# Kernel optimization log

Hardware: AMD Instinct MI355X
Metric: run time of the kernel (lower is better)

The kernel has to match this reference:

```python
import jax, jax.numpy as jnp
import numpy as np

N, E = 40000, 640000
D_IN, D_EDGE, D_HID, D_MSP, D_OUT, L = 16, 8, 128, 256, 4, 2


def _mlp(h, w1, b1, w2, b2):
    # Linear -> ReLU -> Linear
    return jnp.maximum(h @ w1 + b1, 0.0) @ w2 + b2


def setup_inputs() -> dict:
    key = jax.random.key(0)
    ks = jax.random.split(key, 16)
    s = 0.05
    return {
        "x": jax.random.normal(ks[0], (N, D_IN), jnp.float32),
        "edge_attr": jax.random.normal(ks[1], (E, D_EDGE), jnp.float32),
        "edge_index": jax.random.randint(ks[2], (2, E), 0, N, jnp.int32),
        "node_w": jax.random.normal(ks[3], (D_IN, D_HID), jnp.float32) * s,
        "node_b": jnp.zeros((D_HID,), jnp.float32),
        "edge_w": jax.random.normal(ks[4], (D_EDGE, D_HID), jnp.float32) * s,
        "edge_b": jnp.zeros((D_HID,), jnp.float32),
        "msg_w1": jax.random.normal(ks[5], (L, D_HID, D_MSP), jnp.float32) * s,
        "msg_b1": jnp.zeros((L, D_MSP), jnp.float32),
        "msg_w2": jax.random.normal(ks[6], (L, D_MSP, D_HID), jnp.float32) * s,
        "msg_b2": jnp.zeros((L, D_HID), jnp.float32),
        "upd_w1": jax.random.normal(ks[7], (L, D_HID, D_MSP), jnp.float32) * s,
        "upd_b1": jnp.zeros((L, D_MSP), jnp.float32),
        "upd_w2": jax.random.normal(ks[8], (L, D_MSP, D_HID), jnp.float32) * s,
        "upd_b2": jnp.zeros((L, D_HID), jnp.float32),
        "final_w": jax.random.normal(ks[9], (D_HID, D_OUT), jnp.float32) * s,
        "final_b": jnp.zeros((D_OUT,), jnp.float32),
    }


def reference(x, edge_attr, edge_index, node_w, node_b, edge_w, edge_b,
              msg_w1, msg_b1, msg_w2, msg_b2,
              upd_w1, upd_b1, upd_w2, upd_b2, final_w, final_b):
    n_nodes = x.shape[0]
    src, dst = edge_index[0], edge_index[1]  # x_j gathered from src, aggregated onto dst
    # n_lin_layers == 1: single lift layers (dropout is identity in eval)
    h = x @ node_w + node_b                  # [N, 128]
    ea = edge_attr @ edge_w + edge_b         # [E, 128]
    # mean-aggregation degree, zero-degree clamped to 1 (PyG scatter-mean behavior)
    deg = jax.ops.segment_sum(jnp.ones_like(dst, x.dtype), dst, num_segments=n_nodes)
    deg = jnp.maximum(deg, 1.0)[:, None]
    xs = [h]
    for l in range(msg_w1.shape[0]):
        # message: mlp_message(x_j) + mlp_message(edge_attr)
        m = _mlp(h[src], msg_w1[l], msg_b1[l], msg_w2[l], msg_b2[l]) \
            + _mlp(ea, msg_w1[l], msg_b1[l], msg_w2[l], msg_b2[l])
        aggr = jax.ops.segment_sum(m, dst, num_segments=n_nodes) / deg
        # update: mlp_update(x) + mlp_update(aggr_out)
        h = _mlp(h, upd_w1[l], upd_b1[l], upd_w2[l], upd_b2[l]) \
            + _mlp(aggr, upd_w1[l], upd_b1[l], upd_w2[l], upd_b2[l])
        xs.append(h)
    # JumpingKnowledge(mode='max'): elementwise max across layer outputs
    h = jnp.max(jnp.stack(xs, axis=0), axis=0)
    return h @ final_w + final_b  # [N, 4]
```

## Files before the change

kernel.cpp:

```cpp
#include <hip/hip_runtime.h>

#define NN 40000
#define EE 640000
#define MAXT 58752
#define SCAN_B 157

typedef unsigned short u16;
typedef unsigned int u32;
typedef unsigned long long u64;
typedef __attribute__((ext_vector_type(8))) short short8;
typedef __attribute__((ext_vector_type(4))) float f32x4;
typedef __attribute__((ext_vector_type(16))) float f32x16;

__device__ __forceinline__ float bf2f(u16 b){ u32 u=((u32)b)<<16; float f; __builtin_memcpy(&f,&u,4); return f; }
__device__ __forceinline__ u16 f2bf(float f){ u32 u; __builtin_memcpy(&u,&f,4); u = (u + 0x7fffu + ((u>>16)&1u))>>16; return (u16)u; }

#define MFMA __builtin_amdgcn_mfma_f32_16x16x32_bf16
#define MFMA32 __builtin_amdgcn_mfma_f32_32x32x16_bf16

__global__ __launch_bounds__(256)
void packall_kernel(const float* __restrict__ mw1, const float* __restrict__ mw2,
                    const float* __restrict__ uw1, const float* __restrict__ uw2,
                    u16* __restrict__ dm1, u16* __restrict__ dm2,
                    u16* __restrict__ du1, u16* __restrict__ du2){
    int idx = blockIdx.x*blockDim.x + threadIdx.x;
    if (idx >= 4*65536) return;
    int a = idx >> 16, rem = idx & 65535;
    int l = rem >> 15, e = rem & 32767;
    const float* src; u16* dst;
    if (a == 0){ src = mw1; dst = dm1; }
    else if (a == 1){ src = uw1; dst = du1; }
    else if (a == 2){ src = mw2; dst = dm2; }
    else { src = uw2; dst = du2; }
    float v = src[l*32768 + e];
    int o;
    if (a < 2){ int k = e >> 8, n = e & 255;
        o = (((k>>5)*16 + (n>>4))*64 + ((k>>3)&3)*16 + (n&15))*8 + (k&7); }
    else {      int k = e >> 7, n = e & 127;
        o = (((k>>5)*8 + (n>>4))*64 + ((k>>3)&3)*16 + (n&15))*8 + (k&7); }
    dst[l*32768 + o] = f2bf(v);
}

#define SMEM_BYTES 151552

template<int MODE>
__global__ __launch_bounds__(512, 1)
void mlp_kernel(const u16* __restrict__ xa, const u16* __restrict__ xb,
                const u16* __restrict__ w1fg, const float* __restrict__ b1g,
                const u16* __restrict__ w2fg, const float* __restrict__ b2g,
                u16* __restrict__ out16, u16* __restrict__ hmaxb, int ntiles)
{
    extern __shared__ char smem[];
    short8* w1f = (short8*)smem;
    short8* w2f = (short8*)(smem + 65536);
    u16* stg_all = (u16*)(smem + 131072);

    const int tid = threadIdx.x;
    {
        const short8* s1 = (const short8*)w1fg;
        const short8* s2 = (const short8*)w2fg;
        #pragma unroll
        for (int i = 0; i < 8; ++i) w1f[tid + i*512] = s1[tid + i*512];
        #pragma unroll
        for (int i = 0; i < 8; ++i) w2f[tid + i*512] = s2[tid + i*512];
    }
    __syncthreads();

    const int wave = tid >> 6, lane = tid & 63;
    const int g = lane >> 4, c16 = lane & 15;
    u16* stg = stg_all + wave*1280;

    const int wid0 = blockIdx.x*8 + wave;
    const int nwaves = gridDim.x*8;

    for (int t = wid0; t < ntiles; t += nwaves) {
        short8 a[2][4];
        if (MODE == 0) {
            #pragma unroll
            for (int sub = 0; sub < 2; ++sub){
                int r = t*32 + sub*16 + c16;
                #pragma unroll
                for (int kt = 0; kt < 4; ++kt)
                    a[sub][kt] = *(const short8*)(xa + r*128 + kt*32 + g*8);
            }
        } else {
            int r = t*16 + c16;
            #pragma unroll
            for (int kt = 0; kt < 4; ++kt){
                a[0][kt] = *(const short8*)(xa + r*128 + kt*32 + g*8);
                a[1][kt] = *(const short8*)(xb + r*128 + kt*32 + g*8);
            }
        }

        f32x4 oacc[2][8];
        #pragma unroll
        for (int s = 0; s < 2; ++s)
            #pragma unroll
            for (int o = 0; o < 8; ++o) oacc[s][o] = (f32x4){0.f,0.f,0.f,0.f};

        #pragma unroll
        for (int ct = 0; ct < 16; ++ct){
            float bv = b1g[ct*16 + c16];
            f32x4 acc0 = {bv,bv,bv,bv}, acc1 = acc0;
            #pragma unroll
            for (int kt = 0; kt < 4; ++kt){
                short8 b = w1f[(kt*16 + ct)*64 + lane];
                acc0 = MFMA(a[0][kt], b, acc0, 0, 0, 0);
                acc1 = MFMA(a[1][kt], b, acc1, 0, 0, 0);
            }
            int colw = (ct & 1)*16 + c16;
            #pragma unroll
            for (int i = 0; i < 4; ++i){
                int row = g*4 + i;
                stg[row*40 + colw]      = f2bf(fmaxf(acc0[i], 0.f));
                stg[(16+row)*40 + colw] = f2bf(fmaxf(acc1[i], 0.f));
            }
            if (ct & 1){
                int kt2 = ct >> 1;
                short8 a20 = *(const short8*)(stg + c16*40 + g*8);
                short8 a21 = *(const short8*)(stg + (16 + c16)*40 + g*8);
                #pragma unroll
                for (int oc = 0; oc < 8; ++oc){
                    short8 b = w2f[(kt2*8 + oc)*64 + lane];
                    oacc[0][oc] = MFMA(a20, b, oacc[0][oc], 0, 0, 0);
                    oacc[1][oc] = MFMA(a21, b, oacc[1][oc], 0, 0, 0);
                }
            }
        }

        if (MODE == 0) {
            #pragma unroll
            for (int s = 0; s < 2; ++s){
                int rbase = t*32 + s*16 + g*4;
                #pragma unroll
                for (int oc = 0; oc < 8; ++oc){
                    int col = oc*16 + c16; float bb = b2g[col];
                    #pragma unroll
                    for (int i = 0; i < 4; ++i)
                        out16[(rbase + i)*128 + col] = f2bf(oacc[s][oc][i] + bb);
                }
            }
        } else {
            int rbase = t*16 + g*4;
            #pragma unroll
            for (int oc = 0; oc < 8; ++oc){
                int col = oc*16 + c16; float bb2 = 2.f*b2g[col];
                #pragma unroll
                for (int i = 0; i < 4; ++i){
                    float v = oacc[0][oc][i] + oacc[1][oc][i] + bb2;
                    int idx = (rbase + i)*128 + col;
                    float hm = bf2f(hmaxb[idx]);
                    hmaxb[idx] = f2bf(fmaxf(hm, v));
                    out16[idx] = f2bf(v);
                }
            }
        }
    }
}

__global__ __launch_bounds__(512, 1)
void edgeh_kernel(const u16* __restrict__ sea, const u16* __restrict__ tnode,
                  const u16* __restrict__ tne, const int* __restrict__ sbase,
                  const float* __restrict__ W1p, const float* __restrict__ b1p,
                  u16* __restrict__ aggrH)
{
    __shared__ short8 w1f[8*64];
    const int tid = threadIdx.x;
    if (tid < 8*64){
        int cb = tid >> 6, lane = tid & 63, half = lane >> 5, c = lane & 31;
        short8 v = (short8){0,0,0,0,0,0,0,0};
        if (half == 0){
            #pragma unroll
            for (int j = 0; j < 8; ++j) v[j] = (short)f2bf(W1p[j*256 + cb*32 + c]);
        } else {
            v[0] = (short)f2bf(b1p[cb*32 + c]);
        }
        w1f[tid] = v;
    }
    __syncthreads();

    const int wave = tid >> 6, lane = tid & 63;
    const int half = lane >> 5, c32 = lane & 31;
    const int wid0 = blockIdx.x*8 + wave;
    const int nwaves = gridDim.x*8;
    const short8 z = (short8){0,0,0,0,0,0,0,0};
    f32x16 zf16;
    #pragma unroll
    for (int i = 0; i < 16; ++i) zf16[i] = 0.f;

    for (int t = wid0; t < MAXT; t += nwaves){
        u16 tv = tne[t];
        int ne = tv & 0x7fff;
        if (ne == 0) continue;
        bool multi = (tv & 0x8000) != 0;
        int node = tnode[t];
        int sb   = sbase[t];

        bool val = c32 < ne;
        short8 a = z;
        if (half == 0){
            int e = sb + c32; if (e > EE-1) e = EE-1;
            short8 t0 = *(const short8*)(sea + (size_t)e*8);
            a = val ? t0 : z;
        } else {
            a[0] = val ? (short)0x3F80 : (short)0;
        }

        u64 base = (u64)(uintptr_t)(aggrH + (size_t)node*256);
        #pragma unroll
        for (int cb = 0; cb < 8; ++cb){
            short8 b = w1f[cb*64 + lane];
            f32x16 h = MFMA32(a, b, zf16, 0, 0, 0);
            float p0 = fmaxf(h[0],0.f) + fmaxf(h[1],0.f)
                     + fmaxf(h[2],0.f) + fmaxf(h[3],0.f);
            float p1 = fmaxf(h[4],0.f) + fmaxf(h[5],0.f)
                     + fmaxf(h[6],0.f) + fmaxf(h[7],0.f);
            float p2 = fmaxf(h[8],0.f) + fmaxf(h[9],0.f)
                     + fmaxf(h[10],0.f) + fmaxf(h[11],0.f);
            float p3 = fmaxf(h[12],0.f) + fmaxf(h[13],0.f)
                     + fmaxf(h[14],0.f) + fmaxf(h[15],0.f);
            float p = (p0 + p1) + (p2 + p3);
            p += __shfl_xor(p, 32, 64);
            float ph = __shfl_xor(p, 1, 64);
            if (half == 0 && !(c32 & 1)){
                u32 pk;
                asm("v_cvt_pk_bf16_f32 %0, %1, %2" : "=v"(pk) : "v"(p), "v"(ph));
                u64 addr = base + (u64)((cb*32 + c32)*2);
                if (multi){
                    asm volatile("global_atomic_pk_add_bf16 %0, %1, off"
                                 :: "v"(addr), "v"(pk) : "memory");
                } else {
                    *(u32*)(uintptr_t)addr = pk;
                }
            }
        }
    }
}

#define P2_SMEM 135168
__global__ __launch_bounds__(512, 1)
void p2_kernel(const u16* __restrict__ aggrH, const u16* __restrict__ w2fg,
               const float* __restrict__ b2g, const int* __restrict__ deg,
               u16* __restrict__ aggr_bf)
{
    extern __shared__ char smem[];
    short8* w2f = (short8*)smem;
    u16* ostg_all = (u16*)(smem + 65536);
    const int tid = threadIdx.x;
    {
        const short8* s2 = (const short8*)w2fg;
        #pragma unroll
        for (int i = 0; i < 8; ++i) w2f[tid + i*512] = s2[tid + i*512];
    }
    __syncthreads();

    const int wave = tid >> 6, lane = tid & 63;
    const int g = lane >> 4, c16 = lane & 15;
    u16* ostg = ostg_all + wave*(32*136);
    const int wid0 = blockIdx.x*8 + wave;
    const int nwaves = gridDim.x*8;
    const int ntiles = NN/32;

    for (int t = wid0; t < ntiles; t += nwaves){
        short8 a[2][8];
        #pragma unroll
        for (int sub = 0; sub < 2; ++sub){
            int r = t*32 + sub*16 + c16;
            #pragma unroll
            for (int kt = 0; kt < 8; ++kt)
                a[sub][kt] = *(const short8*)(aggrH + (size_t)r*256 + kt*32 + g*8);
        }
        f32x4 acc[2][8];
        #pragma unroll
        for (int s = 0; s < 2; ++s)
            #pragma unroll
            for (int o = 0; o < 8; ++o) acc[s][o] = (f32x4){0.f,0.f,0.f,0.f};
        #pragma unroll
        for (int kt = 0; kt < 8; ++kt){
            #pragma unroll
            for (int oc = 0; oc < 8; ++oc){
                short8 b = w2f[(kt*8 + oc)*64 + lane];
                acc[0][oc] = MFMA(a[0][kt], b, acc[0][oc], 0, 0, 0);
                acc[1][oc] = MFMA(a[1][kt], b, acc[1][oc], 0, 0, 0);
            }
        }
        #pragma unroll
        for (int s = 0; s < 2; ++s){
            int rbase = t*32 + s*16 + g*4;
            float dinv[4]; float tf[4];
            #pragma unroll
            for (int i = 0; i < 4; ++i){
                int d = deg[rbase + i];
                tf[i] = (d > 0) ? 1.f : 0.f;
                dinv[i] = 1.f / (float)((d < 1) ? 1 : d);
            }
            #pragma unroll
            for (int oc = 0; oc < 8; ++oc){
                int col = oc*16 + c16; float bb = b2g[col];
                #pragma unroll
                for (int i = 0; i < 4; ++i){
                    float v = acc[s][oc][i]*dinv[i] + tf[i]*bb;
                    ostg[(s*16 + g*4 + i)*136 + col] = f2bf(v);
                }
            }
        }
        #pragma unroll
        for (int j = 0; j < 8; ++j){
            int flat = j*64 + lane;
            int row = flat >> 4, chunk = flat & 15;
            short8 v = *(const short8*)(ostg + row*136 + chunk*8);
            *(short8*)(aggr_bf + (size_t)(t*32 + row)*128 + chunk*8) = v;
        }
    }
}

__global__ __launch_bounds__(512)
void csr_kernel(const u16* __restrict__ mhb, const u16* __restrict__ ssrc,
                const int* __restrict__ offs, const int* __restrict__ deg,
                u16* __restrict__ aggr_bf)
{
    int w = (int)((blockIdx.x*blockDim.x + threadIdx.x) >> 6);
    int lane = threadIdx.x & 63;
    if (w >= NN) return;
    int o0 = offs[w], dn = deg[w];
    const u32* mh32 = (const u32*)mhb;
    float pl = 0.f, ph = 0.f;
    int k = 0;
    for (; k + 8 <= dn; k += 8){
        u32 v[8];
        #pragma unroll
        for (int j = 0; j < 8; ++j){
            int sc = ssrc[o0 + k + j];
            v[j] = mh32[(size_t)sc*64 + lane];
        }
        #pragma unroll
        for (int j = 0; j < 8; ++j){
            pl += bf2f((u16)(v[j] & 0xffffu));
            ph += bf2f((u16)(v[j] >> 16));
        }
    }
    for (; k < dn; ++k){
        int sc = ssrc[o0+k];
        u32 v = mh32[(size_t)sc*64 + lane];
        pl += bf2f((u16)(v & 0xffffu));
        ph += bf2f((u16)(v >> 16));
    }
    float dinv = 1.f / (float)((dn < 1) ? 1 : dn);
    u32* ab = (u32*)aggr_bf;
    u32 cur = ab[(size_t)w*64 + lane];
    float fl = bf2f((u16)(cur & 0xffffu)) + pl*dinv;
    float fh = bf2f((u16)(cur >> 16))    + ph*dinv;
    ab[(size_t)w*64 + lane] = (u32)f2bf(fl) | ((u32)f2bf(fh) << 16);
}

__global__ void prep_kernel(const float* __restrict__ edge_w, const float* __restrict__ edge_b,
                            const float* __restrict__ msg_w1, const float* __restrict__ msg_b1,
                            float* __restrict__ W1p, float* __restrict__ b1p){
    int l = blockIdx.x, n = threadIdx.x;
    const float* w1 = msg_w1 + l*128*256;
    float acc = msg_b1[l*256 + n];
    for (int c = 0; c < 128; ++c) acc += edge_b[c] * w1[c*256 + n];
    b1p[l*256 + n] = acc;
    #pragma unroll
    for (int k = 0; k < 8; ++k){
        float a = 0.f;
        for (int c = 0; c < 128; ++c) a += edge_w[k*128 + c] * w1[c*256 + n];
        W1p[(l*8 + k)*256 + n] = a;
    }
}

__global__ void lift_kernel(const float* __restrict__ x, const float* __restrict__ nw,
                            const float* __restrict__ nb, u16* __restrict__ hbf,
                            u16* __restrict__ hmaxb){
    int idx = blockIdx.x*blockDim.x + threadIdx.x;
    const int total = NN*128;
    for (; idx < total; idx += gridDim.x*blockDim.x){
        int n = idx >> 7, c = idx & 127;
        const float* xr = x + n*16;
        float acc = nb[c];
        #pragma unroll
        for (int k = 0; k < 16; ++k) acc += xr[k] * nw[k*128 + c];
        u16 hb = f2bf(acc);
        hbf[idx] = hb;
        hmaxb[idx] = hb;
    }
}

__global__ void deg_kernel(const int* __restrict__ eidx, int* __restrict__ deg){
    int i = blockIdx.x*blockDim.x + threadIdx.x;
    for (; i < EE; i += gridDim.x*blockDim.x) atomicAdd(&deg[eidx[EE + i]], 1);
}

__global__ __launch_bounds__(256)
void scanA_kernel(const int* __restrict__ deg, int* __restrict__ partE,
                  int* __restrict__ partT){
    __shared__ int se[256], st[256];
    int t = threadIdx.x;
    int n = blockIdx.x*256 + t;
    int d = (n < NN) ? deg[n] : 0;
    se[t] = d; st[t] = (d + 31) >> 5;
    __syncthreads();
    for (int off = 128; off > 0; off >>= 1){
        if (t < off){ se[t] += se[t+off]; st[t] += st[t+off]; }
        __syncthreads();
    }
    if (t == 0){ partE[blockIdx.x] = se[0]; partT[blockIdx.x] = st[0]; }
}

__global__ __launch_bounds__(256)
void scanB_kernel(int* __restrict__ partE, int* __restrict__ partT){
    __shared__ int pe[256], pt[256];
    int t = threadIdx.x;
    pe[t] = (t < SCAN_B) ? partE[t] : 0;
    pt[t] = (t < SCAN_B) ? partT[t] : 0;
    __syncthreads();
    for (int off = 1; off < 256; off <<= 1){
        int ve = (t >= off) ? pe[t-off] : 0;
        int vt = (t >= off) ? pt[t-off] : 0;
        __syncthreads();
        pe[t] += ve; pt[t] += vt;
        __syncthreads();
    }
    if (t < SCAN_B){ partE[t] = pe[t]; partT[t] = pt[t]; }
}

__global__ __launch_bounds__(256)
void scanC_kernel(const int* __restrict__ deg, const int* __restrict__ partE,
                  const int* __restrict__ partT, int* __restrict__ offs,
                  u16* __restrict__ tnode, u16* __restrict__ tne,
                  int* __restrict__ sbase){
    __shared__ int se[256], st[256];
    int b = blockIdx.x, t = threadIdx.x;
    int n = b*256 + t;
    int d = (n < NN) ? deg[n] : 0;
    int nt = (d + 31) >> 5;
    se[t] = d; st[t] = nt;
    __syncthreads();
    for (int off = 1; off < 256; off <<= 1){
        int ve = (t >= off) ? se[t-off] : 0;
        int vt = (t >= off) ? st[t-off] : 0;
        __syncthreads();
        se[t] += ve; st[t] += vt;
        __syncthreads();
    }
    if (n < NN){
        int rune = ((b > 0) ? partE[b-1] : 0) + se[t] - d;
        int runt = ((b > 0) ? partT[b-1] : 0) + st[t] - nt;
        offs[n] = rune;
        u16 mflag = (nt > 1) ? (u16)0x8000 : (u16)0;
        for (int j = 0; j < nt; ++j){
            int tt = runt + j;
            tnode[tt] = (u16)n;
            int rem = d - 32*j;
            tne[tt] = (u16)(((rem > 32) ? 32 : rem) | mflag);
            sbase[tt] = rune + 32*j;
        }
    }
}

__global__ void place_kernel(const float* __restrict__ eattr, const int* __restrict__ eidx,
                             const int* __restrict__ offs, int* __restrict__ cnt,
                             u16* __restrict__ sea, u16* __restrict__ ssrc){
    int e = blockIdx.x*blockDim.x + threadIdx.x;
    for (; e < EE; e += gridDim.x*blockDim.x){
        int d = eidx[EE + e];
        int pos = offs[d] + atomicAdd(&cnt[d], 1);
        f32x4 a0 = *(const f32x4*)(eattr + (size_t)e*8);
        f32x4 a1 = *(const f32x4*)(eattr + (size_t)e*8 + 4);
        short8 v;
        #pragma unroll
        for (int j = 0; j < 4; ++j){
            v[j]   = (short)f2bf(a0[j]);
            v[4+j] = (short)f2bf(a1[j]);
        }
        *(short8*)(sea + (size_t)pos*8) = v;
        ssrc[pos] = (u16)eidx[e];
    }
}

__global__ void final_kernel(const u16* __restrict__ hmaxb, const float* __restrict__ fw,
                             const float* __restrict__ fb, float* __restrict__ out){
    int t = blockIdx.x*blockDim.x + threadIdx.x;
    if (t >= NN*4) return;
    int n = t >> 2, o = t & 3;
    float acc = fb[o];
    const u16* hr = hmaxb + (size_t)n*128;
    #pragma unroll 16
    for (int c = 0; c < 128; ++c) acc += bf2f(hr[c]) * fw[c*4 + o];
    out[t] = acc;
}

extern "C" void kernel_launch(void* const* d_in, const int* in_sizes, int n_in,
                              void* d_out, int out_size, void* d_ws, size_t ws_size,
                              hipStream_t stream)
{
    (void)in_sizes; (void)n_in; (void)out_size; (void)ws_size;
    const float* x      = (const float*)d_in[0];
    const float* eattr  = (const float*)d_in[1];
    const int*   eidx   = (const int*)d_in[2];
    const float* node_w = (const float*)d_in[3];
    const float* node_b = (const float*)d_in[4];
    const float* edge_w = (const float*)d_in[5];
    const float* edge_b = (const float*)d_in[6];
    const float* msg_w1 = (const float*)d_in[7];
    const float* msg_b1 = (const float*)d_in[8];
    const float* msg_w2 = (const float*)d_in[9];
    const float* msg_b2 = (const float*)d_in[10];
    const float* upd_w1 = (const float*)d_in[11];
    const float* upd_b1 = (const float*)d_in[12];
    const float* upd_w2 = (const float*)d_in[13];
    const float* upd_b2 = (const float*)d_in[14];
    const float* fw     = (const float*)d_in[15];
    const float* fb     = (const float*)d_in[16];
    float* out = (float*)d_out;

    char* ws = (char*)d_ws;
    u16*   hbf     = (u16*)ws;  ws += (size_t)NN*128*2;
    u16*   mhb     = (u16*)ws;  ws += (size_t)NN*128*2;
    u16*   hmaxb   = (u16*)ws;  ws += (size_t)NN*128*2;
    u16*   aggr_bf = (u16*)ws;  ws += (size_t)NN*128*2;
    u16*   aggrH   = (u16*)ws;  ws += (size_t)NN*256*2;
    u16*   sea     = (u16*)ws;  ws += (size_t)EE*8*2;
    u16*   ssrc    = (u16*)ws;  ws += (size_t)EE*2;
    u16*   mw1f    = (u16*)ws;  ws += (size_t)2*32768*2;
    u16*   mw2f    = (u16*)ws;  ws += (size_t)2*32768*2;
    u16*   uw1f    = (u16*)ws;  ws += (size_t)2*32768*2;
    u16*   uw2f    = (u16*)ws;  ws += (size_t)2*32768*2;
    int*   deg     = (int*)ws;  ws += (size_t)NN*4;
    int*   offs    = (int*)ws;  ws += (size_t)NN*4;
    int*   cnt     = (int*)ws;  ws += (size_t)NN*4;
    int*   sbase   = (int*)ws;  ws += (size_t)MAXT*4;
    u16*   tnode   = (u16*)ws;  ws += (size_t)MAXT*2;
    u16*   tne     = (u16*)ws;  ws += (size_t)MAXT*2;
    int*   partE   = (int*)ws;  ws += (size_t)SCAN_B*4;
    int*   partT   = (int*)ws;  ws += (size_t)SCAN_B*4;
    ws = (char*)(((uintptr_t)ws + 15) & ~(uintptr_t)15);
    float* W1p     = (float*)ws; ws += (size_t)2*8*256*4;
    float* b1p     = (float*)ws; ws += (size_t)2*256*4;

    hipFuncSetAttribute(reinterpret_cast<const void*>(&mlp_kernel<0>),
                        hipFuncAttributeMaxDynamicSharedMemorySize, SMEM_BYTES);
    hipFuncSetAttribute(reinterpret_cast<const void*>(&mlp_kernel<1>),
                        hipFuncAttributeMaxDynamicSharedMemorySize, SMEM_BYTES);
    hipFuncSetAttribute(reinterpret_cast<const void*>(&p2_kernel),
                        hipFuncAttributeMaxDynamicSharedMemorySize, P2_SMEM);

    hipMemsetAsync(deg, 0, (size_t)NN*4, stream);
    hipMemsetAsync(cnt, 0, (size_t)NN*4, stream);
    hipMemsetAsync(tne, 0, (size_t)MAXT*2, stream);
    deg_kernel<<<1024, 256, 0, stream>>>(eidx, deg);
    scanA_kernel<<<SCAN_B, 256, 0, stream>>>(deg, partE, partT);
    scanB_kernel<<<1, 256, 0, stream>>>(partE, partT);
    scanC_kernel<<<SCAN_B, 256, 0, stream>>>(deg, partE, partT, offs, tnode, tne, sbase);
    place_kernel<<<1024, 256, 0, stream>>>(eattr, eidx, offs, cnt, sea, ssrc);
    lift_kernel<<<2048, 256, 0, stream>>>(x, node_w, node_b, hbf, hmaxb);
    prep_kernel<<<2, 256, 0, stream>>>(edge_w, edge_b, msg_w1, msg_b1, W1p, b1p);
    packall_kernel<<<1024, 256, 0, stream>>>(msg_w1, msg_w2, upd_w1, upd_w2,
                                             mw1f, mw2f, uw1f, uw2f);

    for (int l = 0; l < 2; ++l){
        mlp_kernel<0><<<256, 512, SMEM_BYTES, stream>>>(
            hbf, nullptr,
            mw1f + l*32768, msg_b1 + l*256, mw2f + l*32768, msg_b2 + l*128,
            mhb, nullptr, NN/32);
        hipMemsetAsync(aggrH, 0, (size_t)NN*256*2, stream);
        edgeh_kernel<<<1024, 512, 0, stream>>>(sea, tnode, tne, sbase,
                                               W1p + l*2048, b1p + l*256, aggrH);
        p2_kernel<<<256, 512, P2_SMEM, stream>>>(aggrH, mw2f + l*32768,
                                                 msg_b2 + l*128, deg, aggr_bf);
        csr_kernel<<<5000, 512, 0, stream>>>(mhb, ssrc, offs, deg, aggr_bf);
        mlp_kernel<1><<<256, 512, SMEM_BYTES, stream>>>(
            hbf, aggr_bf,
            uw1f + l*32768, upd_b1 + l*256, uw2f + l*32768, upd_b2 + l*128,
            hbf, hmaxb, NN/16);
    }

    final_kernel<<<625, 256, 0, stream>>>(hmaxb, fw, fb, out);
}
```

Measured before the change: 415.5 us.

## Permute hidden-column layout so MFMA epilogues write contiguous 16-byte rows

Stores hidden features in a permuted column order (physical p maps to original column (p&7)*16+p>>3), so each lane's eight MFMA output columns are contiguous. The weight packing, node lift and final projection are updated to translate between the two orders. The epilogues of the MLP and p2 kernels now emit short8 vector stores and loads instead of scattered 2-byte accesses. The p2 LDS staging buffer is removed, which lowers its shared memory use and drops the one-block-per-CU bound. The risk is correctness: every consumer of the hidden layout (the edge and CSR kernels, and the second-layer weights) must agree with the new permutation.

```diff
diff --git a/kernel.cpp b/kernel.cpp
--- a/kernel.cpp
+++ b/kernel.cpp
@@ -14,6 +14,8 @@
 
 __device__ __forceinline__ float bf2f(u16 b){ u32 u=((u32)b)<<16; float f; __builtin_memcpy(&f,&u,4); return f; }
 __device__ __forceinline__ u16 f2bf(float f){ u32 u; __builtin_memcpy(&u,&f,4); u = (u + 0x7fffu + ((u>>16)&1u))>>16; return (u16)u; }
+
+__device__ __forceinline__ int origcol(int p){ return ((p & 7) << 4) | (p >> 3); }
 
 #define MFMA __builtin_amdgcn_mfma_f32_16x16x32_bf16
 #define MFMA32 __builtin_amdgcn_mfma_f32_32x32x16_bf16
@@ -32,12 +34,16 @@
     else if (a == 1){ src = uw1; dst = du1; }
     else if (a == 2){ src = mw2; dst = dm2; }
     else { src = uw2; dst = du2; }
-    float v = src[l*32768 + e];
-    int o;
-    if (a < 2){ int k = e >> 8, n = e & 255;
-        o = (((k>>5)*16 + (n>>4))*64 + ((k>>3)&3)*16 + (n&15))*8 + (k&7); }
-    else {      int k = e >> 7, n = e & 127;
-        o = (((k>>5)*8 + (n>>4))*64 + ((k>>3)&3)*16 + (n&15))*8 + (k&7); }
+    float v; int o;
+    if (a < 2){
+        int k = e >> 8, n = e & 255;
+        v = src[l*32768 + origcol(k)*256 + n];
+        o = (((k>>5)*16 + (n>>4))*64 + ((k>>3)&3)*16 + (n&15))*8 + (k&7);
+    } else {
+        int k = e >> 7, n = e & 127;
+        v = src[l*32768 + e];
+        o = (((k>>5)*8 + (n>>4))*64 + ((k>>3)&3)*16 + (n&15))*8 + (k&7);
+    }
     dst[l*32768 + o] = f2bf(v);
 }
 
@@ -133,26 +139,33 @@
             for (int s = 0; s < 2; ++s){
                 int rbase = t*32 + s*16 + g*4;
                 #pragma unroll
-                for (int oc = 0; oc < 8; ++oc){
-                    int col = oc*16 + c16; float bb = b2g[col];
+                for (int i = 0; i < 4; ++i){
+                    short8 v8;
                     #pragma unroll
-                    for (int i = 0; i < 4; ++i)
-                        out16[(rbase + i)*128 + col] = f2bf(oacc[s][oc][i] + bb);
+                    for (int j = 0; j < 8; ++j)
+                        v8[j] = (short)f2bf(oacc[s][j][i] + b2g[j*16 + c16]);
+                    *(short8*)(out16 + (size_t)(rbase + i)*128 + c16*8) = v8;
                 }
             }
         } else {
             int rbase = t*16 + g*4;
             #pragma unroll
-            for (int oc = 0; oc < 8; ++oc){
-                int col = oc*16 + c16; float bb2 = 2.f*b2g[col];
+            for (int i = 0; i < 4; ++i){
+                float vf[8];
+                short8 v8;
                 #pragma unroll
-                for (int i = 0; i < 4; ++i){
-                    float v = oacc[0][oc][i] + oacc[1][oc][i] + bb2;
-                    int idx = (rbase + i)*128 + col;
-                    float hm = bf2f(hmaxb[idx]);
-                    hmaxb[idx] = f2bf(fmaxf(hm, v));
-                    out16[idx] = f2bf(v);
+                for (int j = 0; j < 8; ++j){
+                    vf[j] = oacc[0][j][i] + oacc[1][j][i] + 2.f*b2g[j*16 + c16];
+                    v8[j] = (short)f2bf(vf[j]);
                 }
+                size_t gb = (size_t)(rbase + i)*128 + c16*8;
+                short8 h8 = *(const short8*)(hmaxb + gb);
+                short8 m8;
+                #pragma unroll
+                for (int j = 0; j < 8; ++j)
+                    m8[j] = (short)f2bf(fmaxf(bf2f((u16)h8[j]), vf[j]));
+                *(short8*)(hmaxb + gb) = m8;
+                *(short8*)(out16 + gb) = v8;
             }
         }
     }
@@ -237,15 +250,14 @@
     }
 }
 
-#define P2_SMEM 135168
-__global__ __launch_bounds__(512, 1)
+#define P2_SMEM 65536
+__global__ __launch_bounds__(512)
 void p2_kernel(const u16* __restrict__ aggrH, const u16* __restrict__ w2fg,
                const float* __restrict__ b2g, const int* __restrict__ deg,
                u16* __restrict__ aggr_bf)
 {
     extern __shared__ char smem[];
     short8* w2f = (short8*)smem;
-    u16* ostg_all = (u16*)(smem + 65536);
     const int tid = threadIdx.x;
     {
         const short8* s2 = (const short8*)w2fg;
@@ -256,7 +268,6 @@
 
     const int wave = tid >> 6, lane = tid & 63;
     const int g = lane >> 4, c16 = lane & 15;
-    u16* ostg = ostg_all + wave*(32*136);
     const int wid0 = blockIdx.x*8 + wave;
     const int nwaves = gridDim.x*8;
     const int ntiles = NN/32;
@@ -287,29 +298,17 @@
         #pragma unroll
         for (int s = 0; s < 2; ++s){
             int rbase = t*32 + s*16 + g*4;
-            float dinv[4]; float tf[4];
             #pragma unroll
             for (int i = 0; i < 4; ++i){
                 int d = deg[rbase + i];
-                tf[i] = (d > 0) ? 1.f : 0.f;
-                dinv[i] = 1.f / (float)((d < 1) ? 1 : d);
-            }
-            #pragma unroll
-            for (int oc = 0; oc < 8; ++oc){
-                int col = oc*16 + c16; float bb = b2g[col];
+                float tf = (d > 0) ? 1.f : 0.f;
+                float dinv = 1.f / (float)((d < 1) ? 1 : d);
+                short8 v8;
                 #pragma unroll
-                for (int i = 0; i < 4; ++i){
-                    float v = acc[s][oc][i]*dinv[i] + tf[i]*bb;
-                    ostg[(s*16 + g*4 + i)*136 + col] = f2bf(v);
-                }
-            }
-        }
-        #pragma unroll
-        for (int j = 0; j < 8; ++j){
-            int flat = j*64 + lane;
-            int row = flat >> 4, chunk = flat & 15;
-            short8 v = *(const short8*)(ostg + row*136 + chunk*8);
-            *(short8*)(aggr_bf + (size_t)(t*32 + row)*128 + chunk*8) = v;
+                for (int j = 0; j < 8; ++j)
+                    v8[j] = (short)f2bf(acc[s][j][i]*dinv + tf*b2g[j*16 + c16]);
+                *(short8*)(aggr_bf + (size_t)(rbase + i)*128 + c16*8) = v8;
+            }
         }
     }
 }
@@ -375,7 +374,8 @@
     int idx = blockIdx.x*blockDim.x + threadIdx.x;
     const int total = NN*128;
     for (; idx < total; idx += gridDim.x*blockDim.x){
-        int n = idx >> 7, c = idx & 127;
+        int n = idx >> 7, p = idx & 127;
+        int c = origcol(p);
         const float* xr = x + n*16;
         float acc = nb[c];
         #pragma unroll
@@ -486,7 +486,7 @@
     float acc = fb[o];
     const u16* hr = hmaxb + (size_t)n*128;
     #pragma unroll 16
-    for (int c = 0; c < 128; ++c) acc += bf2f(hr[c]) * fw[c*4 + o];
+    for (int p = 0; p < 128; ++p) acc += bf2f(hr[p]) * fw[origcol(p)*4 + o];
     out[t] = acc;
 }
 
```

Measured after the change: 488.8 us. 1.18x slower.
